# Performance work log

Hardware: AMD Instinct MI355X
Metric: run time of the kernel (lower is better)

Reference implementation:

```python
import jax, jax.numpy as jnp
import numpy as np

B, T, TC, L = 128, 1024, 1024, 4
V, VT, E, H, MAX_OOV = 50000, 50000, 256, 512, 50


def setup_inputs() -> dict:
    key = jax.random.key(0)
    ks = jax.random.split(key, 20)
    s = 0.02
    emb = jax.random.normal(ks[0], (V, E), jnp.float32) * s
    emb = emb.at[0].set(0.0)  # padding_idx=0
    inp = {
        'input_ids': jax.random.randint(ks[1], (B, 1, L), 0, V),
        'h0': jax.random.normal(ks[2], (1, B, H), jnp.float32),
        'c0': jax.random.normal(ks[3], (1, B, H), jnp.float32),
        'encoder_outputs': jax.random.normal(ks[4], (B, T, H), jnp.float32),
        'context_encoder_outputs': jax.random.normal(ks[5], (B, TC, H), jnp.float32),
        'context_input': jax.random.randint(ks[6], (B, TC), 0, VT),
        'emb': emb,
        'W_ih': jax.random.normal(ks[7], (4 * H, E), jnp.float32) * s,
        'W_hh': jax.random.normal(ks[8], (4 * H, H), jnp.float32) * s,
        'b_ih': jnp.zeros((4 * H,), jnp.float32),
        'b_hh': jnp.zeros((4 * H,), jnp.float32),
        'attn_W': jax.random.normal(ks[9], (H, H), jnp.float32) * s,
        'attn_b': jnp.zeros((H,), jnp.float32),
        'cattn_W': jax.random.normal(ks[10], (H, H), jnp.float32) * s,
        'cattn_b': jnp.zeros((H,), jnp.float32),
        'gen_W': jax.random.normal(ks[11], (1, 3 * H + E), jnp.float32) * s,
        'gen_b': jnp.zeros((1,), jnp.float32),
        'sig_b': jax.random.uniform(ks[12], (1,), jnp.float32, -0.1, 0.1),
        'out_W': jax.random.normal(ks[13], (VT, H), jnp.float32) * s,
        'out_b': jnp.zeros((VT,), jnp.float32),
    }
    return inp


def reference(input_ids, h0, c0, encoder_outputs, context_encoder_outputs,
              context_input, emb, W_ih, W_hh, b_ih, b_hh, attn_W, attn_b,
              cattn_W, cattn_b, gen_W, gen_b, sig_b, out_W, out_b):
    # embed: sum subtokens, normalize by l, tanh  -> B,E (input_len == 1)
    l = input_ids.shape[2]
    x = jnp.tanh(emb[input_ids].sum(axis=2) / l)[:, 0, :]  # B,E

    # single LSTM step (PyTorch gate order i,f,g,o)
    h_prev, c_prev = h0[0], c0[0]
    gates = x @ W_ih.T + b_ih + h_prev @ W_hh.T + b_hh  # B,4H
    i, f, g, o = jnp.split(gates, 4, axis=1)
    c_new = jax.nn.sigmoid(f) * c_prev + jax.nn.sigmoid(i) * jnp.tanh(g)
    h_new = jax.nn.sigmoid(o) * jnp.tanh(c_new)
    dec = h_new  # B,H == rnn output squeezed

    # source attention (context_only)
    d1 = dec @ attn_W.T + attn_b
    scores1 = jax.nn.softmax(jnp.einsum('bth,bh->bt', encoder_outputs, d1), axis=1)
    context = jnp.einsum('bt,bth->bh', scores1, encoder_outputs)

    # context attention (score_only) + its context vector
    d2 = dec @ cattn_W.T + cattn_b
    cscores = jax.nn.softmax(jnp.einsum('bth,bh->bt', context_encoder_outputs, d2), axis=1)  # B,TC
    context_context = jnp.einsum('bt,bth->bh', cscores, context_encoder_outputs)

    # generation probability with SigmoidBias
    feat = jnp.concatenate([context, context_context, dec, x], axis=1)  # B,3H+E
    p_gen = jax.nn.sigmoid(feat @ gen_W.T + gen_b + sig_b)  # B,1
    ctx_len = (context_input > 0).sum(axis=1, keepdims=True)
    p_gen = jnp.where(ctx_len == 0, jnp.float32(1.0), p_gen)

    # vocab distribution padded with OOV zeros
    p_vocab = jax.nn.softmax(dec @ out_W.T + out_b, axis=1)
    p_vocab = jnp.concatenate([p_vocab, jnp.zeros((p_vocab.shape[0], MAX_OOV), p_vocab.dtype)], axis=1)

    # copy distribution via scatter-add of attention scores
    Bsz = dec.shape[0]
    p_copy = jnp.zeros((Bsz, VT + MAX_OOV), p_vocab.dtype)
    p_copy = p_copy.at[jnp.arange(Bsz)[:, None], context_input].add(cscores)

    out_prob = p_gen * p_vocab + (1.0 - p_gen) * p_copy
    log_prob = jnp.log(jnp.clip(out_prob, 1e-10))
    return log_prob, h_new[None], c_new[None]
```

## Files before the change

kernel.cpp:

```cpp
#include <hip/hip_runtime.h>


typedef __attribute__((ext_vector_type(8))) short short8;
typedef __attribute__((ext_vector_type(4))) float f32x4;

__device__ __forceinline__ unsigned short f2bf(float x){
  unsigned u = __float_as_uint(x);
  return (unsigned short)((u + 0x7fffu + ((u >> 16) & 1u)) >> 16);
}
__device__ __forceinline__ float sigm(float x){ return 1.f/(1.f+__expf(-x)); }

__global__ __launch_bounds__(256) void k_embed(const int* __restrict__ ids,
    const float* __restrict__ emb, const float* __restrict__ h0,
    float* __restrict__ x_f32, unsigned short* __restrict__ A_lstm){
  int b = blockIdx.x, tid = threadIdx.x;
  int i0 = ids[b*4+0], i1 = ids[b*4+1], i2 = ids[b*4+2], i3 = ids[b*4+3];
  float s = emb[(size_t)i0*256+tid] + emb[(size_t)i1*256+tid]
          + emb[(size_t)i2*256+tid] + emb[(size_t)i3*256+tid];
  float xv = tanhf(s*0.25f);
  x_f32[b*256+tid] = xv;
  A_lstm[b*768+tid] = f2bf(xv);
  for (int j = tid; j < 512; j += 256)
    A_lstm[b*768+256+j] = f2bf(h0[b*512+j]);
}

__global__ __launch_bounds__(256) void gemm_gates(const unsigned short* __restrict__ A,
    const float* __restrict__ Wih, const float* __restrict__ Whh,
    const float* __restrict__ bih, const float* __restrict__ bhh,
    const float* __restrict__ c0, float* __restrict__ out,
    float* __restrict__ dec_f32, unsigned short* __restrict__ dec_bf)
{
  __shared__ union {
    struct { unsigned short As[128*48]; unsigned short Bs[64*48]; } s;
    float gl[4][128][16];
  } u;
  int tid = threadIdx.x, lane = tid & 63, w = tid >> 6;
  int cb = blockIdx.x * 16;
  int mh = (w & 1) * 64, nh = (w >> 1) * 32;
  f32x4 acc[4][2];
  for (int i=0;i<4;i++) for (int j=0;j<2;j++) for (int r=0;r<4;r++) acc[i][j][r]=0.f;

  uint4 ra[2]; float4 rb[2];
  auto loadT = [&](int kk){
    for (int t=0;t<2;t++){
      int s = tid + t*256;
      ra[t] = *(const uint4*)(A + (size_t)(s>>2)*768 + kk + (s&3)*8);
    }
    for (int t=0;t<2;t++){
      int q = tid + t*256; int row = q>>3, kq = q&7;
      int brow = (row>>4)*512 + cb + (row&15);
      const float* p = (kk < 256) ? (Wih + (size_t)brow*256 + kk + kq*4)
                                  : (Whh + (size_t)brow*512 + (kk-256) + kq*4);
      rb[t] = *(const float4*)p;
    }
  };
  loadT(0);
  for (int k0 = 0; k0 < 768; k0 += 32){
    __syncthreads();
    for (int t=0;t<2;t++){
      int s = tid + t*256;
      *(uint4*)(&u.s.As[(s>>2)*48 + (s&3)*8]) = ra[t];
    }
    for (int t=0;t<2;t++){
      int q = tid + t*256; int row = q>>3, kq = q&7;
      unsigned p0 = (unsigned)f2bf(rb[t].x) | ((unsigned)f2bf(rb[t].y) << 16);
      unsigned p1 = (unsigned)f2bf(rb[t].z) | ((unsigned)f2bf(rb[t].w) << 16);
      *(uint2*)(&u.s.Bs[row*48 + kq*4]) = make_uint2(p0, p1);
    }
    __syncthreads();
    if (k0 + 32 < 768) loadT(k0 + 32);
    int kg = (lane >> 4) * 8, lr = lane & 15;
    short8 af[4], bfr[2];
    for (int i=0;i<4;i++) af[i]  = *(const short8*)(&u.s.As[(mh + i*16 + lr)*48 + kg]);
    for (int j=0;j<2;j++) bfr[j] = *(const short8*)(&u.s.Bs[(nh + j*16 + lr)*48 + kg]);
    for (int i=0;i<4;i++)
      for (int j=0;j<2;j++)
        acc[i][j] = __builtin_amdgcn_mfma_f32_16x16x32_bf16(af[i], bfr[j], acc[i][j], 0, 0, 0);
  }
  __syncthreads();
  {
    int lr = lane & 15, q4 = (lane >> 4) * 4;
    for (int j=0;j<2;j++){
      int nl = nh + j*16 + lr;
      int gate = nl >> 4, c = nl & 15;
      int brow = gate*512 + cb + c;
      float bv = bih[brow] + bhh[brow];
      for (int i=0;i<4;i++){
        int m = mh + i*16 + q4;
        for (int r=0;r<4;r++) u.gl[gate][m + r][c] = acc[i][j][r] + bv;
      }
    }
  }
  __syncthreads();
  for (int t = tid; t < 2048; t += 256){
    int m = t >> 4, c = t & 15, col = cb + c;
    float gi = u.gl[0][m][c], gf = u.gl[1][m][c], gg = u.gl[2][m][c], go = u.gl[3][m][c];
    float cc = sigm(gf)*c0[m*512+col] + sigm(gi)*tanhf(gg);
    float h  = sigm(go)*tanhf(cc);
    out[6406400 + m*512 + col] = h;
    out[6406400 + 65536 + m*512 + col] = cc;
    dec_f32[m*512+col] = h;
    dec_bf[m*512+col] = f2bf(h);
  }
}

__global__ __launch_bounds__(256) void gemm128(const unsigned short* __restrict__ A, int lda,
    const float* __restrict__ B0, const float* __restrict__ bias0, float* __restrict__ C0,
    const float* __restrict__ B1, const float* __restrict__ bias1, float* __restrict__ C1,
    int ldc, int N, int K)
{
  const float* Bm  = blockIdx.y ? B1 : B0;
  const float* bias= blockIdx.y ? bias1 : bias0;
  float* C         = blockIdx.y ? C1 : C0;
  __shared__ unsigned short As[128*48];
  __shared__ unsigned short Bs[64*48];
  int tid = threadIdx.x, lane = tid & 63, w = tid >> 6;
  int n0 = blockIdx.x * 64;
  int mh = (w & 1) * 64, nh = (w >> 1) * 32;
  f32x4 acc[4][2];
  for (int i=0;i<4;i++) for (int j=0;j<2;j++) for (int r=0;r<4;r++) acc[i][j][r]=0.f;

  uint4 ra[2]; float4 rb[2];
  auto loadT = [&](int kk){
    for (int t=0;t<2;t++){
      int s = tid + t*256;
      ra[t] = *(const uint4*)(A + (size_t)(s>>2)*lda + kk + (s&3)*8);
    }
    for (int t=0;t<2;t++){
      int q = tid + t*256; int row = q>>3, kq = q&7;
      int n = n0 + row;
      rb[t] = (n < N) ? *(const float4*)(Bm + (size_t)n*K + kk + kq*4)
                      : make_float4(0.f,0.f,0.f,0.f);
    }
  };
  loadT(0);
  for (int k0 = 0; k0 < K; k0 += 32){
    __syncthreads();
    for (int t=0;t<2;t++){
      int s = tid + t*256;
      *(uint4*)(&As[(s>>2)*48 + (s&3)*8]) = ra[t];
    }
    for (int t=0;t<2;t++){
      int q = tid + t*256; int row = q>>3, kq = q&7;
      unsigned p0 = (unsigned)f2bf(rb[t].x) | ((unsigned)f2bf(rb[t].y) << 16);
      unsigned p1 = (unsigned)f2bf(rb[t].z) | ((unsigned)f2bf(rb[t].w) << 16);
      *(uint2*)(&Bs[row*48 + kq*4]) = make_uint2(p0, p1);
    }
    __syncthreads();
    if (k0 + 32 < K) loadT(k0 + 32);
    int kg = (lane >> 4) * 8, lr = lane & 15;
    short8 af[4], bfr[2];
    for (int i=0;i<4;i++) af[i]  = *(const short8*)(&As[(mh + i*16 + lr)*48 + kg]);
    for (int j=0;j<2;j++) bfr[j] = *(const short8*)(&Bs[(nh + j*16 + lr)*48 + kg]);
    for (int i=0;i<4;i++)
      for (int j=0;j<2;j++)
        acc[i][j] = __builtin_amdgcn_mfma_f32_16x16x32_bf16(af[i], bfr[j], acc[i][j], 0, 0, 0);
  }
  int lr = lane & 15, q4 = (lane >> 4) * 4;
  for (int i=0;i<4;i++){
    int mrow = mh + i*16 + q4;
    for (int j=0;j<2;j++){
      int n = n0 + nh + j*16 + lr;
      if (n < N){
        float bv = bias ? bias[n] : 0.f;
        for (int r=0;r<4;r++)
          C[(size_t)(mrow + r)*ldc + n] = acc[i][j][r] + bv;
      }
    }
  }
}

__global__ __launch_bounds__(256) void k_attn(const float* __restrict__ enc,
    const float* __restrict__ cenc, const float* __restrict__ d1v,
    const float* __restrict__ d2v, float* __restrict__ partials,
    float* __restrict__ scraw){
  __shared__ float part[4][514];
  int chunk = blockIdx.x, b = blockIdx.y, z = blockIdx.z;
  const float* src = z ? cenc : enc;
  const float* dv  = z ? d2v : d1v;
  int tid = threadIdx.x, lane = tid & 63, w = tid >> 6;
  const float* dp = dv + b*512 + lane*8;
  float4 da = *(const float4*)dp;
  float4 db = *(const float4*)(dp+4);
  float m = -1e30f, l = 0.f;
  float acc[8];
  #pragma unroll
  for (int i=0;i<8;i++) acc[i]=0.f;
  int t0 = chunk*128 + w*32;
  for (int ti = 0; ti < 32; ti++){
    int t = t0 + ti;
    const float* row = src + ((size_t)b*1024 + t)*512 + lane*8;
    float4 va = *(const float4*)row;
    float4 vb = *(const float4*)(row+4);
    float s = va.x*da.x + va.y*da.y + va.z*da.z + va.w*da.w
            + vb.x*db.x + vb.y*db.y + vb.z*db.z + vb.w*db.w;
    #pragma unroll
    for (int off = 32; off; off >>= 1) s += __shfl_xor(s, off);
    if (z && lane == 0) scraw[b*1024 + t] = s;
    float mn = fmaxf(m, s);
    float alpha = __expf(m - mn);
    float p = __expf(s - mn);
    l = l*alpha + p; m = mn;
    acc[0]=acc[0]*alpha + p*va.x; acc[1]=acc[1]*alpha + p*va.y;
    acc[2]=acc[2]*alpha + p*va.z; acc[3]=acc[3]*alpha + p*va.w;
    acc[4]=acc[4]*alpha + p*vb.x; acc[5]=acc[5]*alpha + p*vb.y;
    acc[6]=acc[6]*alpha + p*vb.z; acc[7]=acc[7]*alpha + p*vb.w;
  }
  #pragma unroll
  for (int i=0;i<8;i++) part[w][lane*8+i] = acc[i];
  if (lane == 0){ part[w][512] = m; part[w][513] = l; }
  __syncthreads();
  float m0=part[0][512], m1=part[1][512], m2=part[2][512], m3=part[3][512];
  float ms = fmaxf(fmaxf(m0,m1), fmaxf(m2,m3));
  float e0=__expf(m0-ms), e1=__expf(m1-ms), e2=__expf(m2-ms), e3=__expf(m3-ms);
  float ls = part[0][513]*e0 + part[1][513]*e1 + part[2][513]*e2 + part[3][513]*e3;
  float* outp = partials + (size_t)((z*128 + b)*8 + chunk)*520;
  for (int j = tid; j < 512; j += 256)
    outp[j] = part[0][j]*e0 + part[1][j]*e1 + part[2][j]*e2 + part[3][j]*e3;
  if (tid == 0){ outp[512] = ms; outp[513] = ls; }
}

__global__ __launch_bounds__(256) void k_acomb_pgen(const float* __restrict__ partials,
    const float* __restrict__ dec, const float* __restrict__ x,
    const float* __restrict__ genW, const float* __restrict__ genb,
    const float* __restrict__ sigb, const int* __restrict__ cin,
    float* __restrict__ mc, float* __restrict__ lc, float* __restrict__ pgen){
  __shared__ float sred[256]; __shared__ int cred[256];
  int b = blockIdx.x, tid = threadIdx.x;
  float p = 0.f;
  for (int z = 0; z < 2; z++){
    const float* base = partials + (size_t)((z*128 + b)*8)*520;
    float ms = -1e30f;
    for (int c=0;c<8;c++) ms = fmaxf(ms, base[c*520+512]);
    float e[8]; float ls = 0.f;
    for (int c=0;c<8;c++){ e[c] = __expf(base[c*520+512]-ms); ls += base[c*520+513]*e[c]; }
    float inv = 1.f/ls;
    for (int j = tid; j < 512; j += 256){
      float s = 0.f;
      for (int c=0;c<8;c++) s += base[c*520+j]*e[c];
      p += s*inv*genW[z*512+j];
    }
    if (z == 1 && tid == 0){ mc[b] = ms; lc[b] = ls; }
  }
  for (int j = tid; j < 512; j += 256) p += dec[b*512+j]*genW[1024+j];
  p += x[b*256+tid]*genW[1536+tid];
  int c = 0;
  for (int t = tid; t < 1024; t += 256) c += (cin[b*1024+t] > 0);
  sred[tid] = p; cred[tid] = c; __syncthreads();
  for (int s2 = 128; s2 > 0; s2 >>= 1){
    if (tid < s2){ sred[tid] += sred[tid+s2]; cred[tid] += cred[tid+s2]; }
    __syncthreads();
  }
  if (tid == 0){
    float pg = sigm(sred[0] + genb[0] + sigb[0]);
    if (cred[0] == 0) pg = 1.f;
    pgen[b] = pg;
  }
}

__global__ __launch_bounds__(256) void k_vstats(const float* __restrict__ logits,
    float* __restrict__ mvp, float* __restrict__ lvp){
  __shared__ float sm[256], sl[256];
  int h = blockIdx.x, b = blockIdx.y, tid = threadIdx.x;
  float m = -1e30f, l = 0.f;
  const float* row = logits + (size_t)b*50000 + h*25000;
  for (int v = tid; v < 25000; v += 256){
    float s = row[v];
    if (s > m){ l = l*__expf(m - s) + 1.f; m = s; }
    else l += __expf(s - m);
  }
  sm[tid] = m; sl[tid] = l; __syncthreads();
  for (int s2 = 128; s2 > 0; s2 >>= 1){
    if (tid < s2){
      float m1 = sm[tid], l1 = sl[tid], m2 = sm[tid+s2], l2 = sl[tid+s2];
      float mn = fmaxf(m1, m2);
      sm[tid] = mn; sl[tid] = l1*__expf(m1-mn) + l2*__expf(m2-mn);
    }
    __syncthreads();
  }
  if (tid == 0){ mvp[b*2+h] = sm[0]; lvp[b*2+h] = sl[0]; }
}

__global__ __launch_bounds__(256) void k_obase(const float* __restrict__ logits,
    const float* __restrict__ mvp, const float* __restrict__ lvp,
    const float* __restrict__ pgen, float* __restrict__ out){
  int b = blockIdx.y;
  int v = blockIdx.x*256 + threadIdx.x;
  if (v >= 50050) return;
  float o;
  if (v < 50000){
    float m0 = mvp[b*2], m1 = mvp[b*2+1], mm = fmaxf(m0, m1);
    float lv = lvp[b*2]*__expf(m0-mm) + lvp[b*2+1]*__expf(m1-mm);
    float pv = __expf(logits[(size_t)b*50000 + v] - mm) / lv;
    o = logf(fmaxf(pgen[b]*pv, 1e-10f));
  } else o = -23.025850929940457f;
  out[(size_t)b*50050 + v] = o;
}

__global__ __launch_bounds__(256) void k_copy(const int* __restrict__ cin,
    const float* __restrict__ scraw, const float* __restrict__ mc,
    const float* __restrict__ lc, const float* __restrict__ logits,
    const float* __restrict__ mvp, const float* __restrict__ lvp,
    const float* __restrict__ pgen, float* __restrict__ pcopy,
    float* __restrict__ out){
  int b = blockIdx.x, tid = threadIdx.x;
  int vv[4];
  #pragma unroll
  for (int t=0;t<4;t++){
    int idx = tid + t*256;
    vv[t] = cin[b*1024 + idx];
    pcopy[(size_t)b*50050 + vv[t]] = 0.f;
  }
  __syncthreads();
  float mb = mc[b], lb = lc[b];
  #pragma unroll
  for (int t=0;t<4;t++){
    int idx = tid + t*256;
    float cs = __expf(scraw[b*1024 + idx] - mb) / lb;
    atomicAdd(&pcopy[(size_t)b*50050 + vv[t]], cs);
  }
  __threadfence();
  __syncthreads();
  float m0 = mvp[b*2], m1 = mvp[b*2+1], mm = fmaxf(m0, m1);
  float lvs = lvp[b*2]*__expf(m0-mm) + lvp[b*2+1]*__expf(m1-mm);
  float pg = pgen[b];
  #pragma unroll
  for (int t=0;t<4;t++){
    int v = vv[t];
    float pv = __expf(logits[(size_t)b*50000 + v] - mm) / lvs;
    float val = pg*pv + (1.f - pg)*pcopy[(size_t)b*50050 + v];
    out[(size_t)b*50050 + v] = logf(fmaxf(val, 1e-10f));
  }
}

extern "C" void kernel_launch(void* const* d_in, const int* in_sizes, int n_in,
                              void* d_out, int out_size, void* d_ws, size_t ws_size,
                              hipStream_t stream){
  const int*   ids  = (const int*)d_in[0];
  const float* h0   = (const float*)d_in[1];
  const float* c0   = (const float*)d_in[2];
  const float* enc  = (const float*)d_in[3];
  const float* cenc = (const float*)d_in[4];
  const int*   cin  = (const int*)d_in[5];
  const float* emb  = (const float*)d_in[6];
  const float* Wih  = (const float*)d_in[7];
  const float* Whh  = (const float*)d_in[8];
  const float* bih  = (const float*)d_in[9];
  const float* bhh  = (const float*)d_in[10];
  const float* attW = (const float*)d_in[11];
  const float* attb = (const float*)d_in[12];
  const float* catW = (const float*)d_in[13];
  const float* catb = (const float*)d_in[14];
  const float* genW = (const float*)d_in[15];
  const float* genb = (const float*)d_in[16];
  const float* sigb = (const float*)d_in[17];
  const float* outW = (const float*)d_in[18];
  const float* outb = (const float*)d_in[19];
  float* out = (float*)d_out;
  char* ws = (char*)d_ws;

  unsigned short* A_lstm  = (unsigned short*)(ws + 0);
  float* x_f32            = (float*)(ws + 196608);
  unsigned short* dec_bf  = (unsigned short*)(ws + 327680);
  float* dec_f32          = (float*)(ws + 458752);
  float* d1               = (float*)(ws + 720896);
  float* d2               = (float*)(ws + 983040);
  float* partials         = (float*)(ws + 1245184);
  float* mc               = (float*)(ws + 5505024);
  float* lc               = (float*)(ws + 5505536);
  float* scraw            = (float*)(ws + 5506048);
  float* pgen             = (float*)(ws + 6030336);
  float* mvp              = (float*)(ws + 6030848);
  float* lvp              = (float*)(ws + 6031872);
  float* logits           = (float*)(ws + 6032896);
  float* pcopy            = (float*)(ws + 31632896);

  hipLaunchKernelGGL(k_embed, dim3(128), dim3(256), 0, stream, ids, emb, h0, x_f32, A_lstm);
  hipLaunchKernelGGL(gemm_gates, dim3(32), dim3(256), 0, stream, A_lstm, Wih, Whh, bih, bhh,
                     c0, out, dec_f32, dec_bf);
  hipLaunchKernelGGL(gemm128, dim3(8,2), dim3(256), 0, stream, dec_bf, 512,
                     attW, attb, d1, catW, catb, d2, 512, 512, 512);
  hipLaunchKernelGGL(gemm128, dim3(782,1), dim3(256), 0, stream, dec_bf, 512,
                     outW, outb, logits, outW, outb, logits, 50000, 50000, 512);
  hipLaunchKernelGGL(k_vstats, dim3(2,128), dim3(256), 0, stream, logits, mvp, lvp);
  hipLaunchKernelGGL(k_attn, dim3(8,128,2), dim3(256), 0, stream, enc, cenc, d1, d2, partials, scraw);
  hipLaunchKernelGGL(k_acomb_pgen, dim3(128), dim3(256), 0, stream, partials, dec_f32, x_f32,
                     genW, genb, sigb, cin, mc, lc, pgen);
  hipLaunchKernelGGL(k_obase, dim3(196,128), dim3(256), 0, stream, logits, mvp, lvp, pgen, out);
  hipLaunchKernelGGL(k_copy, dim3(128), dim3(256), 0, stream, cin, scraw, mc, lc, logits,
                     mvp, lvp, pgen, pcopy, out);
}
```

Before: 822.0 us.

## Fuse vocab GEMM with attention, store bf16 logits, drop max-subtraction in softmaxes

Merges the output-vocab GEMM and both attention passes into one kernel launch, with blocks partitioned by index, so they can run concurrently. Logits are now stored as bf16, which halves the intermediate write and reread traffic. The vocab and attention softmaxes drop running-max tracking and exponentiate raw scores, on the assumption that values stay small. The stats, p_gen and copy-scatter kernels are merged into a single post kernel. The cost is lower logit precision and a risk of overflow if scores ever grow large.

Result: faster. 746.0 us (-9.2%).

```diff
diff --git a/kernel.cpp b/kernel.cpp
--- a/kernel.cpp
+++ b/kernel.cpp
@@ -8,6 +8,8 @@
   unsigned u = __float_as_uint(x);
   return (unsigned short)((u + 0x7fffu + ((u >> 16) & 1u)) >> 16);
 }
+__device__ __forceinline__ float bf2f_lo(unsigned u){ return __uint_as_float(u << 16); }
+__device__ __forceinline__ float bf2f_hi(unsigned u){ return __uint_as_float(u & 0xffff0000u); }
 __device__ __forceinline__ float sigm(float x){ return 1.f/(1.f+__expf(-x)); }
 
 __global__ __launch_bounds__(256) void k_embed(const int* __restrict__ ids,
@@ -170,164 +172,227 @@
   }
 }
 
-__global__ __launch_bounds__(256) void k_attn(const float* __restrict__ enc,
-    const float* __restrict__ cenc, const float* __restrict__ d1v,
-    const float* __restrict__ d2v, float* __restrict__ partials,
-    float* __restrict__ scraw){
-  __shared__ float part[4][514];
-  int chunk = blockIdx.x, b = blockIdx.y, z = blockIdx.z;
-  const float* src = z ? cenc : enc;
-  const float* dv  = z ? d2v : d1v;
+__global__ __launch_bounds__(256) void k_mega(
+    const unsigned short* __restrict__ A,
+    const float* __restrict__ Bm, const float* __restrict__ bias,
+    unsigned short* __restrict__ Cbf,
+    const float* __restrict__ enc, const float* __restrict__ cenc,
+    const float* __restrict__ d1v, const float* __restrict__ d2v,
+    float* __restrict__ partials, float* __restrict__ scraw)
+{
+  __shared__ union {
+    struct { unsigned short As[128*48]; unsigned short Bs[64*48]; } g;
+    float part[4][513];
+  } u;
   int tid = threadIdx.x, lane = tid & 63, w = tid >> 6;
-  const float* dp = dv + b*512 + lane*8;
-  float4 da = *(const float4*)dp;
-  float4 db = *(const float4*)(dp+4);
-  float m = -1e30f, l = 0.f;
-  float acc[8];
-  #pragma unroll
-  for (int i=0;i<8;i++) acc[i]=0.f;
-  int t0 = chunk*128 + w*32;
-  for (int ti = 0; ti < 32; ti++){
-    int t = t0 + ti;
-    const float* row = src + ((size_t)b*1024 + t)*512 + lane*8;
-    float4 va = *(const float4*)row;
-    float4 vb = *(const float4*)(row+4);
-    float s = va.x*da.x + va.y*da.y + va.z*da.z + va.w*da.w
-            + vb.x*db.x + vb.y*db.y + vb.z*db.z + vb.w*db.w;
+  int bid = blockIdx.x;
+  if (bid < 782){
+    const int N = 50000, K = 512;
+    int n0 = bid * 64;
+    int mh = (w & 1) * 64, nh = (w >> 1) * 32;
+    f32x4 acc[4][2];
+    for (int i=0;i<4;i++) for (int j=0;j<2;j++) for (int r=0;r<4;r++) acc[i][j][r]=0.f;
+    uint4 ra[2]; float4 rb[2];
+    auto loadT = [&](int kk){
+      for (int t=0;t<2;t++){
+        int s = tid + t*256;
+        ra[t] = *(const uint4*)(A + (size_t)(s>>2)*512 + kk + (s&3)*8);
+      }
+      for (int t=0;t<2;t++){
+        int q = tid + t*256; int row = q>>3, kq = q&7;
+        int n = n0 + row;
+        rb[t] = (n < N) ? *(const float4*)(Bm + (size_t)n*K + kk + kq*4)
+                        : make_float4(0.f,0.f,0.f,0.f);
+      }
+    };
+    loadT(0);
+    for (int k0 = 0; k0 < K; k0 += 32){
+      __syncthreads();
+      for (int t=0;t<2;t++){
+        int s = tid + t*256;
+        *(uint4*)(&u.g.As[(s>>2)*48 + (s&3)*8]) = ra[t];
+      }
+      for (int t=0;t<2;t++){
+        int q = tid + t*256; int row = q>>3, kq = q&7;
+        unsigned p0 = (unsigned)f2bf(rb[t].x) | ((unsigned)f2bf(rb[t].y) << 16);
+        unsigned p1 = (unsigned)f2bf(rb[t].z) | ((unsigned)f2bf(rb[t].w) << 16);
+        *(uint2*)(&u.g.Bs[row*48 + kq*4]) = make_uint2(p0, p1);
+      }
+      __syncthreads();
+      if (k0 + 32 < K) loadT(k0 + 32);
+      int kg = (lane >> 4) * 8, lr = lane & 15;
+      short8 af[4], bfr[2];
+      for (int i=0;i<4;i++) af[i]  = *(const short8*)(&u.g.As[(mh + i*16 + lr)*48 + kg]);
+      for (int j=0;j<2;j++) bfr[j] = *(const short8*)(&u.g.Bs[(nh + j*16 + lr)*48 + kg]);
+      for (int i=0;i<4;i++)
+        for (int j=0;j<2;j++)
+          acc[i][j] = __builtin_amdgcn_mfma_f32_16x16x32_bf16(af[i], bfr[j], acc[i][j], 0, 0, 0);
+    }
+    int lr = lane & 15, q4 = (lane >> 4) * 4;
+    for (int i=0;i<4;i++){
+      int mrow = mh + i*16 + q4;
+      for (int j=0;j<2;j++){
+        int n = n0 + nh + j*16 + lr;
+        if (n < N){
+          float bv = bias[n];
+          for (int r=0;r<4;r++)
+            Cbf[(size_t)(mrow + r)*50000 + n] = f2bf(acc[i][j][r] + bv);
+        }
+      }
+    }
+  } else {
+    int a = bid - 782;
+    int chunk = a & 7, b = (a >> 3) & 127, z = a >> 10;
+    const float* src = z ? cenc : enc;
+    const float* dv  = z ? d2v : d1v;
+    const float* dp = dv + b*512 + lane*8;
+    float4 da = *(const float4*)dp;
+    float4 db = *(const float4*)(dp+4);
+    float l = 0.f;
+    float acc[8];
     #pragma unroll
-    for (int off = 32; off; off >>= 1) s += __shfl_xor(s, off);
-    if (z && lane == 0) scraw[b*1024 + t] = s;
-    float mn = fmaxf(m, s);
-    float alpha = __expf(m - mn);
-    float p = __expf(s - mn);
-    l = l*alpha + p; m = mn;
-    acc[0]=acc[0]*alpha + p*va.x; acc[1]=acc[1]*alpha + p*va.y;
-    acc[2]=acc[2]*alpha + p*va.z; acc[3]=acc[3]*alpha + p*va.w;
-    acc[4]=acc[4]*alpha + p*vb.x; acc[5]=acc[5]*alpha + p*vb.y;
-    acc[6]=acc[6]*alpha + p*vb.z; acc[7]=acc[7]*alpha + p*vb.w;
-  }
-  #pragma unroll
-  for (int i=0;i<8;i++) part[w][lane*8+i] = acc[i];
-  if (lane == 0){ part[w][512] = m; part[w][513] = l; }
-  __syncthreads();
-  float m0=part[0][512], m1=part[1][512], m2=part[2][512], m3=part[3][512];
-  float ms = fmaxf(fmaxf(m0,m1), fmaxf(m2,m3));
-  float e0=__expf(m0-ms), e1=__expf(m1-ms), e2=__expf(m2-ms), e3=__expf(m3-ms);
-  float ls = part[0][513]*e0 + part[1][513]*e1 + part[2][513]*e2 + part[3][513]*e3;
-  float* outp = partials + (size_t)((z*128 + b)*8 + chunk)*520;
-  for (int j = tid; j < 512; j += 256)
-    outp[j] = part[0][j]*e0 + part[1][j]*e1 + part[2][j]*e2 + part[3][j]*e3;
-  if (tid == 0){ outp[512] = ms; outp[513] = ls; }
-}
-
-__global__ __launch_bounds__(256) void k_acomb_pgen(const float* __restrict__ partials,
+    for (int i=0;i<8;i++) acc[i]=0.f;
+    int t0 = chunk*128 + w*32;
+    const float* base = src + ((size_t)b*1024 + t0)*512 + lane*8;
+    #pragma unroll 4
+    for (int ti = 0; ti < 32; ti++){
+      const float* row = base + (size_t)ti*512;
+      float4 va = *(const float4*)row;
+      float4 vb = *(const float4*)(row+4);
+      float s = va.x*da.x + va.y*da.y + va.z*da.z + va.w*da.w
+              + vb.x*db.x + vb.y*db.y + vb.z*db.z + vb.w*db.w;
+      #pragma unroll
+      for (int off = 32; off; off >>= 1) s += __shfl_xor(s, off);
+      float p = __expf(s);
+      if (z && lane == 0) scraw[b*1024 + t0 + ti] = s;
+      l += p;
+      acc[0] += p*va.x; acc[1] += p*va.y; acc[2] += p*va.z; acc[3] += p*va.w;
+      acc[4] += p*vb.x; acc[5] += p*vb.y; acc[6] += p*vb.z; acc[7] += p*vb.w;
+    }
+    #pragma unroll
+    for (int i=0;i<8;i++) u.part[w][lane*8+i] = acc[i];
+    if (lane == 0) u.part[w][512] = l;
+    __syncthreads();
+    float* outp = partials + (size_t)((z*128 + b)*8 + chunk)*516;
+    for (int j = tid; j < 512; j += 256)
+      outp[j] = u.part[0][j] + u.part[1][j] + u.part[2][j] + u.part[3][j];
+    if (tid == 0)
+      outp[512] = u.part[0][512] + u.part[1][512] + u.part[2][512] + u.part[3][512];
+  }
+}
+
+__global__ __launch_bounds__(256) void k_post1(const float* __restrict__ partials,
     const float* __restrict__ dec, const float* __restrict__ x,
     const float* __restrict__ genW, const float* __restrict__ genb,
     const float* __restrict__ sigb, const int* __restrict__ cin,
-    float* __restrict__ mc, float* __restrict__ lc, float* __restrict__ pgen){
-  __shared__ float sred[256]; __shared__ int cred[256];
-  int b = blockIdx.x, tid = threadIdx.x;
-  float p = 0.f;
-  for (int z = 0; z < 2; z++){
-    const float* base = partials + (size_t)((z*128 + b)*8)*520;
-    float ms = -1e30f;
-    for (int c=0;c<8;c++) ms = fmaxf(ms, base[c*520+512]);
-    float e[8]; float ls = 0.f;
-    for (int c=0;c<8;c++){ e[c] = __expf(base[c*520+512]-ms); ls += base[c*520+513]*e[c]; }
-    float inv = 1.f/ls;
-    for (int j = tid; j < 512; j += 256){
-      float s = 0.f;
-      for (int c=0;c<8;c++) s += base[c*520+j]*e[c];
-      p += s*inv*genW[z*512+j];
-    }
-    if (z == 1 && tid == 0){ mc[b] = ms; lc[b] = ls; }
-  }
-  for (int j = tid; j < 512; j += 256) p += dec[b*512+j]*genW[1024+j];
-  p += x[b*256+tid]*genW[1536+tid];
-  int c = 0;
-  for (int t = tid; t < 1024; t += 256) c += (cin[b*1024+t] > 0);
-  sred[tid] = p; cred[tid] = c; __syncthreads();
-  for (int s2 = 128; s2 > 0; s2 >>= 1){
-    if (tid < s2){ sred[tid] += sred[tid+s2]; cred[tid] += cred[tid+s2]; }
-    __syncthreads();
-  }
-  if (tid == 0){
-    float pg = sigm(sred[0] + genb[0] + sigb[0]);
-    if (cred[0] == 0) pg = 1.f;
-    pgen[b] = pg;
-  }
-}
-
-__global__ __launch_bounds__(256) void k_vstats(const float* __restrict__ logits,
-    float* __restrict__ mvp, float* __restrict__ lvp){
-  __shared__ float sm[256], sl[256];
-  int h = blockIdx.x, b = blockIdx.y, tid = threadIdx.x;
-  float m = -1e30f, l = 0.f;
-  const float* row = logits + (size_t)b*50000 + h*25000;
-  for (int v = tid; v < 25000; v += 256){
-    float s = row[v];
-    if (s > m){ l = l*__expf(m - s) + 1.f; m = s; }
-    else l += __expf(s - m);
-  }
-  sm[tid] = m; sl[tid] = l; __syncthreads();
-  for (int s2 = 128; s2 > 0; s2 >>= 1){
-    if (tid < s2){
-      float m1 = sm[tid], l1 = sl[tid], m2 = sm[tid+s2], l2 = sl[tid+s2];
-      float mn = fmaxf(m1, m2);
-      sm[tid] = mn; sl[tid] = l1*__expf(m1-mn) + l2*__expf(m2-mn);
-    }
-    __syncthreads();
-  }
-  if (tid == 0){ mvp[b*2+h] = sm[0]; lvp[b*2+h] = sl[0]; }
-}
-
-__global__ __launch_bounds__(256) void k_obase(const float* __restrict__ logits,
-    const float* __restrict__ mvp, const float* __restrict__ lvp,
-    const float* __restrict__ pgen, float* __restrict__ out){
+    const unsigned short* __restrict__ logits_bf, const float* __restrict__ scraw,
+    float* __restrict__ lvp, float* __restrict__ pgen, float* __restrict__ pcopy)
+{
+  int bid = blockIdx.x, tid = threadIdx.x;
+  if (bid < 256){
+    __shared__ float sl[256];
+    int b = bid >> 1, h = bid & 1;
+    const unsigned short* row = logits_bf + (size_t)b*50000 + h*25000;
+    float l = 0.f;
+    for (int v = tid; v < 3125; v += 256){
+      uint4 q = *(const uint4*)(row + v*8);
+      l += __expf(bf2f_lo(q.x)) + __expf(bf2f_hi(q.x));
+      l += __expf(bf2f_lo(q.y)) + __expf(bf2f_hi(q.y));
+      l += __expf(bf2f_lo(q.z)) + __expf(bf2f_hi(q.z));
+      l += __expf(bf2f_lo(q.w)) + __expf(bf2f_hi(q.w));
+    }
+    sl[tid] = l; __syncthreads();
+    for (int s2 = 128; s2 > 0; s2 >>= 1){
+      if (tid < s2) sl[tid] += sl[tid+s2];
+      __syncthreads();
+    }
+    if (tid == 0) lvp[b*2+h] = sl[0];
+  } else if (bid < 384){
+    __shared__ float sred[256]; __shared__ int cred[256];
+    int b = bid - 256;
+    float p = 0.f;
+    for (int z = 0; z < 2; z++){
+      const float* base = partials + (size_t)((z*128 + b)*8)*516;
+      float ls = 0.f;
+      for (int c=0;c<8;c++) ls += base[c*516+512];
+      float inv = 1.f/ls;
+      for (int j = tid; j < 512; j += 256){
+        float s = 0.f;
+        for (int c=0;c<8;c++) s += base[c*516+j];
+        p += s*inv*genW[z*512+j];
+      }
+    }
+    for (int j = tid; j < 512; j += 256) p += dec[b*512+j]*genW[1024+j];
+    p += x[b*256+tid]*genW[1536+tid];
+    int c = 0;
+    for (int t = tid; t < 1024; t += 256) c += (cin[b*1024+t] > 0);
+    sred[tid] = p; cred[tid] = c; __syncthreads();
+    for (int s2 = 128; s2 > 0; s2 >>= 1){
+      if (tid < s2){ sred[tid] += sred[tid+s2]; cred[tid] += cred[tid+s2]; }
+      __syncthreads();
+    }
+    if (tid == 0){
+      float pg = sigm(sred[0] + genb[0] + sigb[0]);
+      if (cred[0] == 0) pg = 1.f;
+      pgen[b] = pg;
+    }
+  } else {
+    int b = bid - 384;
+    float lc = 0.f;
+    const float* basep = partials + (size_t)((128 + b)*8)*516;
+    for (int c=0;c<8;c++) lc += basep[c*516+512];
+    float inv = 1.f/lc;
+    int vv[4];
+    #pragma unroll
+    for (int t=0;t<4;t++){
+      int idx = tid + t*256;
+      vv[t] = cin[b*1024 + idx];
+      pcopy[(size_t)b*50050 + vv[t]] = 0.f;
+    }
+    __syncthreads();
+    #pragma unroll
+    for (int t=0;t<4;t++){
+      int idx = tid + t*256;
+      float cs = __expf(scraw[b*1024 + idx]) * inv;
+      atomicAdd(&pcopy[(size_t)b*50050 + vv[t]], cs);
+    }
+  }
+}
+
+__global__ __launch_bounds__(256) void k_obase(const unsigned short* __restrict__ logits_bf,
+    const float* __restrict__ lvp, const float* __restrict__ pgen,
+    float* __restrict__ out){
   int b = blockIdx.y;
-  int v = blockIdx.x*256 + threadIdx.x;
-  if (v >= 50050) return;
-  float o;
-  if (v < 50000){
-    float m0 = mvp[b*2], m1 = mvp[b*2+1], mm = fmaxf(m0, m1);
-    float lv = lvp[b*2]*__expf(m0-mm) + lvp[b*2+1]*__expf(m1-mm);
-    float pv = __expf(logits[(size_t)b*50000 + v] - mm) / lv;
-    o = logf(fmaxf(pgen[b]*pv, 1e-10f));
-  } else o = -23.025850929940457f;
-  out[(size_t)b*50050 + v] = o;
-}
-
-__global__ __launch_bounds__(256) void k_copy(const int* __restrict__ cin,
-    const float* __restrict__ scraw, const float* __restrict__ mc,
-    const float* __restrict__ lc, const float* __restrict__ logits,
-    const float* __restrict__ mvp, const float* __restrict__ lvp,
-    const float* __restrict__ pgen, float* __restrict__ pcopy,
+  int v0 = (blockIdx.x*256 + threadIdx.x) * 2;
+  if (v0 >= 50050) return;
+  float2 res;
+  if (v0 < 50000){
+    float lv = lvp[b*2] + lvp[b*2+1];
+    float pg = pgen[b];
+    unsigned q = *(const unsigned*)(logits_bf + (size_t)b*50000 + v0);
+    float inv = pg / lv;
+    res.x = logf(fmaxf(__expf(bf2f_lo(q)) * inv, 1e-10f));
+    res.y = logf(fmaxf(__expf(bf2f_hi(q)) * inv, 1e-10f));
+  } else {
+    res.x = -23.025850929940457f;
+    res.y = -23.025850929940457f;
+  }
+  *(float2*)(out + (size_t)b*50050 + v0) = res;
+}
+
+__global__ __launch_bounds__(256) void k_cfix(const int* __restrict__ cin,
+    const float* __restrict__ pcopy, const unsigned short* __restrict__ logits_bf,
+    const float* __restrict__ lvp, const float* __restrict__ pgen,
     float* __restrict__ out){
   int b = blockIdx.x, tid = threadIdx.x;
-  int vv[4];
+  float lv = lvp[b*2] + lvp[b*2+1];
+  float pg = pgen[b];
   #pragma unroll
   for (int t=0;t<4;t++){
     int idx = tid + t*256;
-    vv[t] = cin[b*1024 + idx];
-    pcopy[(size_t)b*50050 + vv[t]] = 0.f;
-  }
-  __syncthreads();
-  float mb = mc[b], lb = lc[b];
-  #pragma unroll
-  for (int t=0;t<4;t++){
-    int idx = tid + t*256;
-    float cs = __expf(scraw[b*1024 + idx] - mb) / lb;
-    atomicAdd(&pcopy[(size_t)b*50050 + vv[t]], cs);
-  }
-  __threadfence();
-  __syncthreads();
-  float m0 = mvp[b*2], m1 = mvp[b*2+1], mm = fmaxf(m0, m1);
-  float lvs = lvp[b*2]*__expf(m0-mm) + lvp[b*2+1]*__expf(m1-mm);
-  float pg = pgen[b];
-  #pragma unroll
-  for (int t=0;t<4;t++){
-    int v = vv[t];
-    float pv = __expf(logits[(size_t)b*50000 + v] - mm) / lvs;
+    int v = cin[b*1024 + idx];
+    float logit = __uint_as_float(((unsigned)logits_bf[(size_t)b*50000 + v]) << 16);
+    float pv = __expf(logit) / lv;
     float val = pg*pv + (1.f - pg)*pcopy[(size_t)b*50050 + v];
     out[(size_t)b*50050 + v] = logf(fmaxf(val, 1e-10f));
   }
@@ -359,34 +424,28 @@
   float* out = (float*)d_out;
   char* ws = (char*)d_ws;
 
-  unsigned short* A_lstm  = (unsigned short*)(ws + 0);
-  float* x_f32            = (float*)(ws + 196608);
-  unsigned short* dec_bf  = (unsigned short*)(ws + 327680);
-  float* dec_f32          = (float*)(ws + 458752);
-  float* d1               = (float*)(ws + 720896);
-  float* d2               = (float*)(ws + 983040);
-  float* partials         = (float*)(ws + 1245184);
-  float* mc               = (float*)(ws + 5505024);
-  float* lc               = (float*)(ws + 5505536);
-  float* scraw            = (float*)(ws + 5506048);
-  float* pgen             = (float*)(ws + 6030336);
-  float* mvp              = (float*)(ws + 6030848);
-  float* lvp              = (float*)(ws + 6031872);
-  float* logits           = (float*)(ws + 6032896);
-  float* pcopy            = (float*)(ws + 31632896);
+  unsigned short* A_lstm   = (unsigned short*)(ws + 0);
+  float* x_f32             = (float*)(ws + 196608);
+  unsigned short* dec_bf   = (unsigned short*)(ws + 327680);
+  float* dec_f32           = (float*)(ws + 458752);
+  float* d1                = (float*)(ws + 720896);
+  float* d2                = (float*)(ws + 983040);
+  float* partials          = (float*)(ws + 1245184);
+  float* scraw             = (float*)(ws + 5472256);
+  float* pgen              = (float*)(ws + 5996544);
+  float* lvp               = (float*)(ws + 5997056);
+  unsigned short* logitsbf = (unsigned short*)(ws + 5998080);
+  float* pcopy             = (float*)(ws + 18798080);
 
   hipLaunchKernelGGL(k_embed, dim3(128), dim3(256), 0, stream, ids, emb, h0, x_f32, A_lstm);
   hipLaunchKernelGGL(gemm_gates, dim3(32), dim3(256), 0, stream, A_lstm, Wih, Whh, bih, bhh,
                      c0, out, dec_f32, dec_bf);
   hipLaunchKernelGGL(gemm128, dim3(8,2), dim3(256), 0, stream, dec_bf, 512,
                      attW, attb, d1, catW, catb, d2, 512, 512, 512);
-  hipLaunchKernelGGL(gemm128, dim3(782,1), dim3(256), 0, stream, dec_bf, 512,
-                     outW, outb, logits, outW, outb, logits, 50000, 50000, 512);
-  hipLaunchKernelGGL(k_vstats, dim3(2,128), dim3(256), 0, stream, logits, mvp, lvp);
-  hipLaunchKernelGGL(k_attn, dim3(8,128,2), dim3(256), 0, stream, enc, cenc, d1, d2, partials, scraw);
-  hipLaunchKernelGGL(k_acomb_pgen, dim3(128), dim3(256), 0, stream, partials, dec_f32, x_f32,
-                     genW, genb, sigb, cin, mc, lc, pgen);
-  hipLaunchKernelGGL(k_obase, dim3(196,128), dim3(256), 0, stream, logits, mvp, lvp, pgen, out);
-  hipLaunchKernelGGL(k_copy, dim3(128), dim3(256), 0, stream, cin, scraw, mc, lc, logits,
-                     mvp, lvp, pgen, pcopy, out);
-}
+  hipLaunchKernelGGL(k_mega, dim3(2830), dim3(256), 0, stream, dec_bf, outW, outb, logitsbf,
+                     enc, cenc, d1, d2, partials, scraw);
+  hipLaunchKernelGGL(k_post1, dim3(512), dim3(256), 0, stream, partials, dec_f32, x_f32,
+                     genW, genb, sigb, cin, logitsbf, scraw, lvp, pgen, pcopy);
+  hipLaunchKernelGGL(k_obase, dim3(98,128), dim3(256), 0, stream, logitsbf, lvp, pgen, out);
+  hipLaunchKernelGGL(k_cfix, dim3(128), dim3(256), 0, stream, cin, pcopy, logitsbf, lvp, pgen, out);
+}
```
